# Performance work log

Measured on AMD Instinct MI355X. Metric: run time of the kernel, lower is better.

Reference implementation:

```python
import jax, jax.numpy as jnp
import numpy as np

B, S, D, H, DK, DFF, L = 4, 1024, 1024, 16, 64, 4096, 128

def setup_inputs() -> dict:
    key = jax.random.key(0)
    ks = jax.random.split(key, 20)
    stdv = 1.0 / np.sqrt(D)
    u = lambda k, shape, s=stdv: jax.random.uniform(k, shape, jnp.float32, -s, s)
    x = jax.random.normal(ks[0], (B, S, D), jnp.float32)
    causal = jnp.triu(jnp.ones((S, S), bool), 1)          # True = masked
    attn_mask = jnp.broadcast_to(causal, (B, S, S))
    return {
        "x": x,
        "attn_mask": attn_mask,
        "W_q": u(ks[1], (H * DK, D)), "b_q": jnp.zeros((H * DK,)),
        "W_k": u(ks[2], (H * DK, D)), "b_k": jnp.zeros((H * DK,)),
        "W_v": u(ks[3], (H * DK, D)), "b_v": jnp.zeros((H * DK,)),
        "W_o": u(ks[4], (D, H * DK)), "b_o": jnp.zeros((D,)),
        "W_rel": u(ks[5], (2 * L + 1, DK), 1.0 / np.sqrt(DK)),
        "ln1_alpha": jnp.ones((D,)), "ln1_bias": jnp.zeros((D,)),
        "ln2_alpha": jnp.ones((D,)), "ln2_bias": jnp.zeros((D,)),
        "W1": u(ks[6], (DFF, D)), "b1": jnp.zeros((DFF,)),
        "W2": u(ks[7], (D, DFF)), "b2": jnp.zeros((D,)),
    }

def _layer_norm(x, alpha, bias, eps=1e-5):
    # Faithful to source: (x - mean) / (std + eps), std is biased (unbiased=False)
    m = jnp.mean(x, axis=-1, keepdims=True)
    std = jnp.sqrt(jnp.mean((x - m) ** 2, axis=-1, keepdims=True))
    return alpha * (x - m) / (std + eps) + bias

def reference(x, attn_mask, W_q, b_q, W_k, b_k, W_v, b_v, W_o, b_o, W_rel,
              ln1_alpha, ln1_bias, ln2_alpha, ln2_bias, W1, b1, W2, b2):
    b, s, d = x.shape
    q = (x @ W_q.T + b_q).reshape(b, s, H, DK)
    k = (x @ W_k.T + b_k).reshape(b, s, H, DK)
    v = (x @ W_v.T + b_v).reshape(b, s, H, DK)
    # relative position bias table lookup -> [s, s, DK]
    idx = jnp.clip(jnp.arange(s)[:, None] - jnp.arange(s)[None, :], -L, L) + L
    pos = W_rel[idx]
    # NOTE: original uses rel_pos_k_emb for BOTH pos_key and pos_value (as in source).
    scores = jnp.einsum('bqnd,bknd->bnqk', q, k) + jnp.einsum('bqnd,qkd->bnqk', q, pos)
    scores = scores / np.sqrt(DK)
    scores = jnp.where(attn_mask[:, None, :, :], jnp.float32(-10000.0), scores)
    attn = jax.nn.softmax(scores, axis=-1)
    out = jnp.einsum('bnqk,bknd->bnqd', attn, v) + jnp.einsum('bnqk,qkd->bnqd', attn, pos)
    out = out.transpose(0, 2, 1, 3).reshape(b, s, H * DK)
    out = out @ W_o.T + b_o
    # post-LN transformer layer: LN(x + attn), then LN(h + FFN(h))
    h = _layer_norm(x + out, ln1_alpha, ln1_bias)
    f = jax.nn.relu(h @ W1.T + b1) @ W2.T + b2
    return _layer_norm(h + f, ln2_alpha, ln2_bias)
```

## Files before the change

kernel.cpp:

```cpp
#include <hip/hip_runtime.h>
#include <cmath>
#include <cstdint>

typedef __bf16 bf16;
typedef __bf16 bf16x8 __attribute__((ext_vector_type(8)));
typedef __bf16 bf16x4 __attribute__((ext_vector_type(4)));
typedef float f32x4 __attribute__((ext_vector_type(4)));

#define CEXP 0.1803368852f

__device__ __forceinline__ void async_ld16(const void* g, void* l) {
  __builtin_amdgcn_global_load_lds(
      (__attribute__((address_space(1))) void*)(uintptr_t)g,
      (__attribute__((address_space(3))) void*)l, 16, 0, 0);
}

__global__ __launch_bounds__(256) void cast_all(
    const float* __restrict__ x,  const float* __restrict__ wq, const float* __restrict__ wk,
    const float* __restrict__ wv, const float* __restrict__ wo, const float* __restrict__ w1,
    const float* __restrict__ w2,
    bf16* xb, bf16* wqb, bf16* wkb, bf16* wvb, bf16* wob, bf16* w1b, bf16* w2b)
{
  int i = blockIdx.x * 256 + threadIdx.x;
  const int M1 = 1 << 20, Q = 1 << 18;
  const float* src; bf16* dst; int off;
  if      (i < M1)            { src = x;  dst = xb;  off = i; }
  else if (i < M1 + Q)        { src = wq; dst = wqb; off = i - M1; }
  else if (i < M1 + 2 * Q)    { src = wk; dst = wkb; off = i - M1 - Q; }
  else if (i < M1 + 3 * Q)    { src = wv; dst = wvb; off = i - M1 - 2 * Q; }
  else if (i < M1 + 4 * Q)    { src = wo; dst = wob; off = i - M1 - 3 * Q; }
  else if (i < 3 * M1)        { src = w1; dst = w1b; off = i - M1 - 4 * Q; }
  else                        { src = w2; dst = w2b; off = i - 3 * M1; }
  float4 v = ((const float4*)src)[off];
  bf16x4 o; o[0]=(bf16)v.x; o[1]=(bf16)v.y; o[2]=(bf16)v.z; o[3]=(bf16)v.w;
  ((bf16x4*)dst)[off] = o;
}

template<int BM>
__device__ __forceinline__ void gemm_core(
    const bf16* __restrict__ A, const bf16* __restrict__ Bm, const float* __restrict__ bias,
    float* __restrict__ outF, bf16* __restrict__ outB,
    const float* __restrict__ residF, const bf16* __restrict__ residB,
    int N, int kld, int kbeg, int kend, int relu, bf16* As, bf16* Bs)
{
  constexpr int MI = BM / 32;
  const int tid  = threadIdx.x;
  const int wave = tid >> 6, lane = tid & 63;
  const int lr = lane & 15, lq = lane >> 4;
  const int bm = blockIdx.x * BM, bn = blockIdx.y * 128;
  const int wm = (wave >> 1) * (BM / 2), wn = (wave & 1) * 64;
  const int srow = lane >> 2, scol = (lane & 3) * 8;

  const f32x4 fz = {0.f, 0.f, 0.f, 0.f};
  f32x4 acc[MI][4];
#pragma unroll
  for (int i = 0; i < MI; i++)
#pragma unroll
    for (int j = 0; j < 4; j++) acc[i][j] = fz;

  auto issue = [&](int k0, int buf) {
    bf16* Ad = As + buf * (BM * 32);
    bf16* Bd = Bs + buf * (128 * 32);
    if (BM == 128) {
#pragma unroll
      for (int cc = 0; cc < 2; ++cc) {
        int c = wave * 2 + cc;
        async_ld16(A + (size_t)(bm + c * 16 + srow) * kld + k0 + scol, Ad + c * 512);
      }
    } else {
      async_ld16(A + (size_t)(bm + wave * 16 + srow) * kld + k0 + scol, Ad + wave * 512);
    }
#pragma unroll
    for (int cc = 0; cc < 2; ++cc) {
      int c = wave * 2 + cc;
      async_ld16(Bm + (size_t)(bn + c * 16 + srow) * kld + k0 + scol, Bd + c * 512);
    }
  };

  const int nit = (kend - kbeg) >> 5;
  issue(kbeg, 0);
  for (int i = 0; i < nit; i++) {
    __syncthreads();
    if (i + 1 < nit) issue(kbeg + (i + 1) * 32, (i + 1) & 1);
    const bf16* Ab = As + (i & 1) * (BM * 32);
    const bf16* Bb = Bs + (i & 1) * (128 * 32);
    bf16x8 af[MI], bfr[4];
#pragma unroll
    for (int mi = 0; mi < MI; mi++) af[mi]  = *(const bf16x8*)(Ab + (wm + mi*16 + lr)*32 + lq*8);
#pragma unroll
    for (int ni = 0; ni < 4; ni++) bfr[ni] = *(const bf16x8*)(Bb + (wn + ni*16 + lr)*32 + lq*8);
#pragma unroll
    for (int mi = 0; mi < MI; mi++)
#pragma unroll
      for (int ni = 0; ni < 4; ni++)
        acc[mi][ni] = __builtin_amdgcn_mfma_f32_16x16x32_bf16(af[mi], bfr[ni], acc[mi][ni], 0, 0, 0);
  }

#pragma unroll
  for (int ni = 0; ni < 4; ni++) {
    int n = bn + wn + ni*16 + lr;
    float bv = bias ? bias[n] : 0.0f;
#pragma unroll
    for (int mi = 0; mi < MI; mi++) {
#pragma unroll
      for (int r = 0; r < 4; r++) {
        int m = bm + wm + mi*16 + lq*4 + r;
        size_t idx = (size_t)m * N + n;
        float v = acc[mi][ni][r] + bv;
        if (relu) v = fmaxf(v, 0.0f);
        if (residF) v += residF[idx];
        if (residB) v += (float)residB[idx];
        if (outF) outF[idx] = v;
        else      outB[idx] = (bf16)v;
      }
    }
  }
}

__global__ __launch_bounds__(256) void gemm_qkv(
    const bf16* A, const bf16* Bq, const bf16* Bk, const bf16* Bv,
    const float* bq, const float* bk, const float* bv,
    bf16* Oq, bf16* Ok, bf16* Ov, int N, int K)
{
  __shared__ bf16 As[2 * 128 * 32];
  __shared__ bf16 Bs[2 * 128 * 32];
  const bf16* Bm  = blockIdx.z == 0 ? Bq : (blockIdx.z == 1 ? Bk : Bv);
  const float* bi = blockIdx.z == 0 ? bq : (blockIdx.z == 1 ? bk : bv);
  bf16* O         = blockIdx.z == 0 ? Oq : (blockIdx.z == 1 ? Ok : Ov);
  gemm_core<128>(A, Bm, bi, nullptr, O, nullptr, nullptr, N, K, 0, K, 0, As, Bs);
}

__device__ __forceinline__ void gemm256_core(
    const bf16* __restrict__ A, const bf16* __restrict__ Bm,
    const float* __restrict__ bias, bf16* __restrict__ outB, float* __restrict__ outF,
    int N, int kld, int kbeg, int kend, int relu, bf16* As, bf16* Bs)
{
  const int tid  = threadIdx.x;
  const int wave = tid >> 6, lane = tid & 63;
  const int lr = lane & 15, lq = lane >> 4;
  const int bm = blockIdx.x * 256, bn = blockIdx.y * 256;
  const int wm = (wave >> 2) * 128, wn = (wave & 3) * 64;

  const f32x4 fz = {0.f, 0.f, 0.f, 0.f};
  f32x4 acc[8][4];
#pragma unroll
  for (int i = 0; i < 8; ++i)
#pragma unroll
    for (int j = 0; j < 4; ++j) acc[i][j] = fz;

  int srow[4], scol[4];
#pragma unroll
  for (int L = 0; L < 4; ++L) {
    int cidx = L * 512 + wave * 64 + lane;
    srow[L] = cidx >> 3;
    scol[L] = ((cidx & 7) ^ (srow[L] & 7)) * 8;
  }

  auto issue = [&](int kt, int buf) {
    const int k0 = kbeg + kt * 64;
#pragma unroll
    for (int L = 0; L < 4; ++L)
      async_ld16(A + (size_t)(bm + srow[L]) * kld + k0 + scol[L],
                 As + buf * (256 * 64) + (L * 512 + wave * 64) * 8);
#pragma unroll
    for (int L = 0; L < 4; ++L)
      async_ld16(Bm + (size_t)(bn + srow[L]) * kld + k0 + scol[L],
                 Bs + buf * (256 * 64) + (L * 512 + wave * 64) * 8);
  };

  const int NT = (kend - kbeg) >> 6;
  issue(0, 0);
  issue(1, 1);
  asm volatile("s_waitcnt vmcnt(8)" ::: "memory");
  __builtin_amdgcn_sched_barrier(0);
  __builtin_amdgcn_s_barrier();

  for (int t = 0; t < NT; ++t) {
    const bf16* Ab = As + (t & 1) * (256 * 64);
    const bf16* Bb = Bs + (t & 1) * (256 * 64);
#pragma unroll
    for (int mh = 0; mh < 2; ++mh) {
      bf16x8 af[4][2];
#pragma unroll
      for (int mi = 0; mi < 4; ++mi) {
        int row = wm + mh * 64 + mi * 16 + lr;
#pragma unroll
        for (int ks = 0; ks < 2; ++ks)
          af[mi][ks] = *(const bf16x8*)(Ab + row * 64 + (((ks * 4 + lq) ^ (lr & 7)) * 8));
      }
#pragma unroll
      for (int nh = 0; nh < 2; ++nh) {
        bf16x8 bfr[2][2];
#pragma unroll
        for (int ni = 0; ni < 2; ++ni) {
          int row = wn + nh * 32 + ni * 16 + lr;
#pragma unroll
          for (int ks = 0; ks < 2; ++ks)
            bfr[ni][ks] = *(const bf16x8*)(Bb + row * 64 + (((ks * 4 + lq) ^ (lr & 7)) * 8));
        }
        __builtin_amdgcn_s_setprio(1);
#pragma unroll
        for (int mi = 0; mi < 4; ++mi)
#pragma unroll
          for (int ni = 0; ni < 2; ++ni)
#pragma unroll
            for (int ks = 0; ks < 2; ++ks)
              acc[mh * 4 + mi][nh * 2 + ni] = __builtin_amdgcn_mfma_f32_16x16x32_bf16(
                  af[mi][ks], bfr[ni][ks], acc[mh * 4 + mi][nh * 2 + ni], 0, 0, 0);
        __builtin_amdgcn_s_setprio(0);
      }
    }
    if (t + 1 == NT) break;
    asm volatile("s_waitcnt lgkmcnt(0)" ::: "memory");
    __builtin_amdgcn_sched_barrier(0);
    __builtin_amdgcn_s_barrier();
    if (t + 2 < NT) {
      issue(t + 2, t & 1);
      asm volatile("s_waitcnt vmcnt(8)" ::: "memory");
    } else {
      asm volatile("s_waitcnt vmcnt(0)" ::: "memory");
    }
    __builtin_amdgcn_sched_barrier(0);
    __builtin_amdgcn_s_barrier();
  }

#pragma unroll
  for (int mi8 = 0; mi8 < 8; ++mi8) {
#pragma unroll
    for (int ni4 = 0; ni4 < 4; ++ni4) {
      int n = bn + wn + ni4 * 16 + lr;
      float bv = bias ? bias[n] : 0.0f;
#pragma unroll
      for (int r = 0; r < 4; ++r) {
        int m = bm + wm + mi8 * 16 + lq * 4 + r;
        size_t idx = (size_t)m * N + n;
        float v = acc[mi8][ni4][r] + bv;
        if (relu) v = fmaxf(v, 0.0f);
        if (outF) outF[idx] = v;
        else      outB[idx] = (bf16)v;
      }
    }
  }
}

__global__ __launch_bounds__(512) void gemm256(
    const bf16* __restrict__ A, const bf16* __restrict__ Bm,
    const float* __restrict__ bias, bf16* __restrict__ outB,
    int N, int K, int relu)
{
  __shared__ __align__(16) bf16 As[2 * 256 * 64];
  __shared__ __align__(16) bf16 Bs[2 * 256 * 64];
  gemm256_core(A, Bm, bias, outB, nullptr, N, K, 0, K, relu, As, Bs);
}

__device__ __forceinline__ void gemm256x128_core(
    const bf16* __restrict__ A, const bf16* __restrict__ Bm, float* __restrict__ outF,
    int N, int kld, int kbeg, int kend, bf16* As, bf16* Bs)
{
  const int tid  = threadIdx.x;
  const int wave = tid >> 6, lane = tid & 63;
  const int lr = lane & 15, lq = lane >> 4;
  const int bm = blockIdx.x * 256, bn = blockIdx.y * 128;
  const int wm = (wave >> 1) * 64, wn = (wave & 1) * 64;

  const f32x4 fz = {0.f, 0.f, 0.f, 0.f};
  f32x4 acc[4][4];
#pragma unroll
  for (int i = 0; i < 4; ++i)
#pragma unroll
    for (int j = 0; j < 4; ++j) acc[i][j] = fz;

  int srowA[4], scolA[4], srowB[2], scolB[2];
#pragma unroll
  for (int L = 0; L < 4; ++L) {
    int cidx = L * 512 + wave * 64 + lane;
    srowA[L] = cidx >> 3;
    scolA[L] = ((cidx & 7) ^ (srowA[L] & 7)) * 8;
  }
#pragma unroll
  for (int L = 0; L < 2; ++L) {
    int cidx = L * 512 + wave * 64 + lane;
    srowB[L] = cidx >> 3;
    scolB[L] = ((cidx & 7) ^ (srowB[L] & 7)) * 8;
  }

  auto issue = [&](int kt, int buf) {
    const int k0 = kbeg + kt * 64;
#pragma unroll
    for (int L = 0; L < 4; ++L)
      async_ld16(A + (size_t)(bm + srowA[L]) * kld + k0 + scolA[L],
                 As + buf * (256 * 64) + (L * 512 + wave * 64) * 8);
#pragma unroll
    for (int L = 0; L < 2; ++L)
      async_ld16(Bm + (size_t)(bn + srowB[L]) * kld + k0 + scolB[L],
                 Bs + buf * (128 * 64) + (L * 512 + wave * 64) * 8);
  };

  const int NT = (kend - kbeg) >> 6;
  issue(0, 0);
  issue(1, 1);
  asm volatile("s_waitcnt vmcnt(6)" ::: "memory");
  __builtin_amdgcn_sched_barrier(0);
  __builtin_amdgcn_s_barrier();

  for (int t = 0; t < NT; ++t) {
    const bf16* Ab = As + (t & 1) * (256 * 64);
    const bf16* Bb = Bs + (t & 1) * (128 * 64);
    bf16x8 af[4][2], bfr[4][2];
#pragma unroll
    for (int mi = 0; mi < 4; ++mi) {
      int row = wm + mi * 16 + lr;
#pragma unroll
      for (int ks = 0; ks < 2; ++ks)
        af[mi][ks] = *(const bf16x8*)(Ab + row * 64 + (((ks * 4 + lq) ^ (lr & 7)) * 8));
    }
#pragma unroll
    for (int ni = 0; ni < 4; ++ni) {
      int row = wn + ni * 16 + lr;
#pragma unroll
      for (int ks = 0; ks < 2; ++ks)
        bfr[ni][ks] = *(const bf16x8*)(Bb + row * 64 + (((ks * 4 + lq) ^ (lr & 7)) * 8));
    }
    __builtin_amdgcn_s_setprio(1);
#pragma unroll
    for (int mi = 0; mi < 4; ++mi)
#pragma unroll
      for (int ni = 0; ni < 4; ++ni)
#pragma unroll
        for (int ks = 0; ks < 2; ++ks)
          acc[mi][ni] = __builtin_amdgcn_mfma_f32_16x16x32_bf16(
              af[mi][ks], bfr[ni][ks], acc[mi][ni], 0, 0, 0);
    __builtin_amdgcn_s_setprio(0);

    if (t + 1 == NT) break;
    asm volatile("s_waitcnt lgkmcnt(0)" ::: "memory");
    __builtin_amdgcn_sched_barrier(0);
    __builtin_amdgcn_s_barrier();
    if (t + 2 < NT) {
      issue(t + 2, t & 1);
      asm volatile("s_waitcnt vmcnt(6)" ::: "memory");
    } else {
      asm volatile("s_waitcnt vmcnt(0)" ::: "memory");
    }
    __builtin_amdgcn_sched_barrier(0);
    __builtin_amdgcn_s_barrier();
  }

#pragma unroll
  for (int mi = 0; mi < 4; ++mi) {
#pragma unroll
    for (int ni = 0; ni < 4; ++ni) {
      int n = bn + wn + ni * 16 + lr;
#pragma unroll
      for (int r = 0; r < 4; ++r) {
        int m = bm + wm + mi * 16 + lq * 4 + r;
        outF[(size_t)m * N + n] = acc[mi][ni][r];
      }
    }
  }
}

__global__ __launch_bounds__(512) void gemm256x128_splitk(
    const bf16* __restrict__ A, const bf16* __restrict__ Bm,
    float* p0, float* p1, int N, int kld, int kchunk)
{
  __shared__ __align__(16) bf16 As[2 * 256 * 64];
  __shared__ __align__(16) bf16 Bs[2 * 128 * 64];
  const int z = blockIdx.z;
  float* part = z == 0 ? p0 : p1;
  gemm256x128_core(A, Bm, part, N, kld, z * kchunk, (z + 1) * kchunk, As, Bs);
}

__global__ __launch_bounds__(256) void transpose_v(const bf16* __restrict__ V, bf16* __restrict__ Vt) {
  __shared__ bf16 t[64][72];
  const int tid = threadIdx.x;
  const int sblk = blockIdx.x;
  const int bh = blockIdx.y;
  const int b = bh >> 4, h = bh & 15;
  const int sr = tid >> 2, dc = (tid & 3) * 16;
  const bf16* src = V + ((size_t)(b * 1024 + sblk * 64 + sr)) * 1024 + h * 64 + dc;
  bf16x8 r0 = *(const bf16x8*)src;
  bf16x8 r1 = *(const bf16x8*)(src + 8);
  *(bf16x8*)(&t[sr][dc]) = r0;
  *(bf16x8*)(&t[sr][dc + 8]) = r1;
  __syncthreads();
  const int dr = tid >> 2, sc = (tid & 3) * 16;
  bf16 o[16];
#pragma unroll
  for (int j = 0; j < 16; j++) o[j] = t[sc + j][dr];
  bf16* dst = Vt + ((size_t)(bh * 64 + dr)) * 1024 + sblk * 64 + sc;
  *(bf16x8*)dst = *(bf16x8*)&o[0];
  *(bf16x8*)(dst + 8) = *(bf16x8*)&o[8];
}

#define S_LEN 1024
#define ROWSTR 1024

__global__ __launch_bounds__(256) void attn_kernel(
    const bf16* __restrict__ Qg, const bf16* __restrict__ Kg, const bf16* __restrict__ Vt,
    const float* __restrict__ Wrel, bf16* __restrict__ Og)
{
  __shared__ __align__(16) bf16 hist[64][136];
  __shared__ __align__(16) bf16 rel_s[64][132];
  __shared__ __align__(16) bf16 ovl[8704];
  bf16* V_T  = ovl;
  bf16* Pb   = ovl + 4096;
  bf16* Wst  = ovl;
  bf16* Wr_t = ovl;
  float* lbuf = (float*)rel_s;
  float* hbuf = lbuf + 256;

  const int tid = threadIdx.x;
  const int wave = tid >> 6, lane = tid & 63;
  const int lr = lane & 15, lq = lane >> 4;
  const int qblk = 15 - blockIdx.y;
  const int bh = blockIdx.x;
  const int b = bh >> 4, h = bh & 15;
  const int q0 = qblk * 64;
  const int T = qblk + 1;
  const int nearStart = (T > 3) ? T - 3 : 0;
  const size_t rowbase = (size_t)b * S_LEN * ROWSTR + h * 64;
  const size_t vtbase = (size_t)(bh * 64) * 1024;
  const f32x4 fz = {0.f, 0.f, 0.f, 0.f};

  for (int e = tid; e < 2048; e += 256) {
    float4 v = ((const float4*)(Wrel + 8192))[e];
    bf16x4 o; o[0]=(bf16)v.x; o[1]=(bf16)v.y; o[2]=(bf16)v.z; o[3]=(bf16)v.w;
    ((bf16x4*)Wst)[e] = o;
  }
  {
    uint4 z4 = {0u, 0u, 0u, 0u};
    for (int e = tid; e < 1088; e += 256) ((uint4*)hist)[e] = z4;
  }

  bf16x8 qf[4][2];
#pragma unroll
  for (int qt = 0; qt < 4; qt++)
#pragma unroll
    for (int c = 0; c < 2; c++)
      qf[qt][c] = *(const bf16x8*)(Qg + rowbase + (size_t)(q0 + qt*16 + lr) * ROWSTR + c*32 + lq*8);

  bf16x8 wb[2];
#pragma unroll
  for (int c = 0; c < 2; c++)
#pragma unroll
    for (int j = 0; j < 8; j++)
      wb[c][j] = (bf16)Wrel[(size_t)256 * 64 + c*32 + lq*8 + j];

  __syncthreads();

#pragma unroll
  for (int tt = 0; tt < 2; ++tt)
#pragma unroll
    for (int qt = 0; qt < 4; ++qt) {
      f32x4 a = fz;
#pragma unroll
      for (int c = 0; c < 2; c++) {
        bf16x8 wf = *(const bf16x8*)(Wst + (wave*32 + tt*16 + lr) * 64 + c*32 + lq*8);
        a = __builtin_amdgcn_mfma_f32_16x16x32_bf16(wf, qf[qt][c], a, 0, 0, 0);
      }
      bf16x4 pk; pk[0]=(bf16)(a[0]*CEXP); pk[1]=(bf16)(a[1]*CEXP);
                 pk[2]=(bf16)(a[2]*CEXP); pk[3]=(bf16)(a[3]*CEXP);
      *(bf16x4*)(&rel_s[qt*16 + lr][wave*32 + tt*16 + lq*4]) = pk;
    }
  {
    f32x4 a = fz;
#pragma unroll
    for (int c = 0; c < 2; c++)
      a = __builtin_amdgcn_mfma_f32_16x16x32_bf16(wb[c], qf[wave][c], a, 0, 0, 0);
    if (lq == 0) rel_s[wave*16 + lr][128] = (bf16)(a[0]*CEXP);
  }
  __syncthreads();

  float relc[4];
#pragma unroll
  for (int qt = 0; qt < 4; qt++) relc[qt] = (float)rel_s[qt*16 + lr][128];

  float l_p[4] = {0.f,0.f,0.f,0.f}, h_p[4] = {0.f,0.f,0.f,0.f};
  f32x4 acc_o[4];
#pragma unroll
  for (int dt = 0; dt < 4; dt++) acc_o[dt] = fz;

  const int vd1 = tid >> 3;
  const int vj  = (tid & 7) ^ (vd1 & 7);
  const int krow = 16 * wave + lr;

  uint4 va, vb, va2, vb2;
  bf16x8 kf0, kf1, kn0, kn1;
  {
    const bf16* vp = Vt + vtbase + (size_t)vd1 * 1024 + vj * 8;
    va = *(const uint4*)vp; vb = *(const uint4*)(vp + 32 * 1024);
    const bf16* kp = Kg + rowbase + (size_t)krow * ROWSTR + lq*8;
    kf0 = *(const bf16x8*)kp; kf1 = *(const bf16x8*)(kp + 32);
  }

  for (int kt = 0; kt < T; ++kt) {
    const int k0 = kt * 64;

    f32x4 sc[4];
#pragma unroll
    for (int qt = 0; qt < 4; qt++) {
      sc[qt] = __builtin_amdgcn_mfma_f32_16x16x32_bf16(kf0, qf[qt][0], fz, 0, 0, 0);
      sc[qt] = __builtin_amdgcn_mfma_f32_16x16x32_bf16(kf1, qf[qt][1], sc[qt], 0, 0, 0);
    }
    if (kt + 1 < T) {
      const bf16* vp = Vt + vtbase + (size_t)vd1 * 1024 + k0 + 64 + vj * 8;
      va2 = *(const uint4*)vp; vb2 = *(const uint4*)(vp + 32 * 1024);
      const bf16* kp = Kg + rowbase + (size_t)(k0 + 64 + krow) * ROWSTR + lq*8;
      kn0 = *(const bf16x8*)kp; kn1 = *(const bf16x8*)(kp + 32);
    }

    float pw[4][4];
    if (kt < nearStart) {
#pragma unroll
      for (int qt = 0; qt < 4; qt++) {
#pragma unroll
        for (int r = 0; r < 4; r++) pw[qt][r] = exp2f(fmaf(sc[qt][r], CEXP, relc[qt]));
        float s4 = pw[qt][0] + pw[qt][1] + pw[qt][2] + pw[qt][3];
        l_p[qt] += s4; h_p[qt] += s4;
      }
    } else {
#pragma unroll
      for (int qt = 0; qt < 4; qt++) {
        int qg = q0 + qt*16 + lr;
#pragma unroll
        for (int r = 0; r < 4; r++) {
          int kg = k0 + 16*wave + lq*4 + r;
          float p = 0.0f;
          if (kg <= qg) {
            int t = qg - kg; int tc = t > 128 ? 128 : t;
            p = exp2f(fmaf(sc[qt][r], CEXP, (float)rel_s[qt*16 + lr][tc]));
            l_p[qt] += p;
            if (t >= 128) h_p[qt] += p;
            else          hist[qt*16 + lr][t] = (bf16)p;
          }
          pw[qt][r] = p;
        }
      }
    }

    __syncthreads();
    *(uint4*)(V_T + tid * 8) = va;
    *(uint4*)(V_T + (tid + 256) * 8) = vb;
#pragma unroll
    for (int qt = 0; qt < 4; qt++) {
      bf16x4 pk; pk[0]=(bf16)pw[qt][0]; pk[1]=(bf16)pw[qt][1];
                 pk[2]=(bf16)pw[qt][2]; pk[3]=(bf16)pw[qt][3];
      *(bf16x4*)(Pb + (qt*16 + lr) * 72 + 16*wave + lq*4) = pk;
    }
    __syncthreads();

#pragma unroll
    for (int c = 0; c < 2; c++) {
      bf16x8 pf = *(const bf16x8*)(Pb + (16*wave + lr) * 72 + c*32 + lq*8);
#pragma unroll
      for (int dt = 0; dt < 4; dt++) {
        int vd = dt*16 + lr;
        int jx = (c*4 + lq) ^ (vd & 7);
        bf16x8 vf = *(const bf16x8*)(V_T + ((vd << 3) + jx) * 8);
        acc_o[dt] = __builtin_amdgcn_mfma_f32_16x16x32_bf16(pf, vf, acc_o[dt], 0, 0, 0);
      }
    }
    kf0 = kn0; kf1 = kn1; va = va2; vb = vb2;
  }

#pragma unroll
  for (int qt = 0; qt < 4; qt++) {
    l_p[qt] += __shfl_xor(l_p[qt], 16); l_p[qt] += __shfl_xor(l_p[qt], 32);
    h_p[qt] += __shfl_xor(h_p[qt], 16); h_p[qt] += __shfl_xor(h_p[qt], 32);
  }
  __syncthreads();
  if (lq == 0) {
#pragma unroll
    for (int qt = 0; qt < 4; qt++) {
      lbuf[wave*64 + qt*16 + lr] = l_p[qt];
      hbuf[wave*64 + qt*16 + lr] = h_p[qt];
    }
  }
  for (int e = tid; e < 64 * 128; e += 256) {
    int d = e >> 7, t = e & 127;
    Wr_t[d * 136 + t] = (bf16)Wrel[(size_t)(128 + t) * 64 + d];
  }
  __syncthreads();
#pragma unroll
  for (int c = 0; c < 4; c++) {
    bf16x8 hf = *(const bf16x8*)&hist[wave*16 + lr][c*32 + lq*8];
#pragma unroll
    for (int dt = 0; dt < 4; dt++) {
      bf16x8 wf = *(const bf16x8*)(Wr_t + (dt*16 + lr) * 136 + c*32 + lq*8);
      acc_o[dt] = __builtin_amdgcn_mfma_f32_16x16x32_bf16(hf, wf, acc_o[dt], 0, 0, 0);
    }
  }
  float l4[4], h4[4];
#pragma unroll
  for (int r = 0; r < 4; r++) {
    int q = wave*16 + lq*4 + r;
    l4[r] = lbuf[q] + lbuf[64+q] + lbuf[128+q] + lbuf[192+q];
    h4[r] = hbuf[q] + hbuf[64+q] + hbuf[128+q] + hbuf[192+q];
  }
#pragma unroll
  for (int dt = 0; dt < 4; dt++) {
    float wv = Wrel[(size_t)256 * 64 + dt*16 + lr];
#pragma unroll
    for (int r = 0; r < 4; r++) acc_o[dt][r] += h4[r] * wv;
  }
#pragma unroll
  for (int dt = 0; dt < 4; dt++)
#pragma unroll
    for (int r = 0; r < 4; r++) {
      int qg = q0 + wave*16 + lq*4 + r;
      Og[rowbase + (size_t)qg * ROWSTR + dt*16 + lr] = (bf16)(acc_o[dt][r] / l4[r]);
    }
}

__global__ __launch_bounds__(256) void ln_fuse(
    const float* __restrict__ pA, const float* __restrict__ pB,
    const float* __restrict__ pC, const float* __restrict__ pD,
    const float* __restrict__ bias,
    const float* __restrict__ residF, const bf16* __restrict__ residB,
    const float* __restrict__ alpha, const float* __restrict__ beta,
    float* __restrict__ outF, bf16* __restrict__ outB)
{
  const int row = blockIdx.x, tid = threadIdx.x;
  const int lane = tid & 63, wave = tid >> 6;
  const size_t base = (size_t)row * 1024;
  float4 v = ((const float4*)(pA + base))[tid];
  float4 v2 = ((const float4*)(pB + base))[tid];
  v.x += v2.x; v.y += v2.y; v.z += v2.z; v.w += v2.w;
  if (pC) {
    float4 v3 = ((const float4*)(pC + base))[tid];
    v.x += v3.x; v.y += v3.y; v.z += v3.z; v.w += v3.w;
  }
  if (pD) {
    float4 v4 = ((const float4*)(pD + base))[tid];
    v.x += v4.x; v.y += v4.y; v.z += v4.z; v.w += v4.w;
  }
  float4 bv = ((const float4*)bias)[tid];
  v.x += bv.x; v.y += bv.y; v.z += bv.z; v.w += bv.w;
  if (residF) {
    float4 rv = ((const float4*)(residF + base))[tid];
    v.x += rv.x; v.y += rv.y; v.z += rv.z; v.w += rv.w;
  }
  if (residB) {
    bf16x4 rv = ((const bf16x4*)(residB + base))[tid];
    v.x += (float)rv[0]; v.y += (float)rv[1]; v.z += (float)rv[2]; v.w += (float)rv[3];
  }
  float s  = v.x + v.y + v.z + v.w;
  float ss = v.x*v.x + v.y*v.y + v.z*v.z + v.w*v.w;
#pragma unroll
  for (int off = 32; off; off >>= 1) { s += __shfl_down(s, off); ss += __shfl_down(ss, off); }
  __shared__ float rs[4], rss[4];
  if (lane == 0) { rs[wave] = s; rss[wave] = ss; }
  __syncthreads();
  s  = rs[0] + rs[1] + rs[2] + rs[3];
  ss = rss[0] + rss[1] + rss[2] + rss[3];
  float mean = s * (1.0f / 1024.0f);
  float var  = ss * (1.0f / 1024.0f) - mean * mean;
  float inv  = 1.0f / (sqrtf(fmaxf(var, 0.0f)) + 1e-5f);
  float4 a = ((const float4*)alpha)[tid];
  float4 bb = ((const float4*)beta)[tid];
  float o0 = a.x * (v.x - mean) * inv + bb.x;
  float o1 = a.y * (v.y - mean) * inv + bb.y;
  float o2 = a.z * (v.z - mean) * inv + bb.z;
  float o3 = a.w * (v.w - mean) * inv + bb.w;
  if (outF) { float4 o = {o0, o1, o2, o3}; ((float4*)(outF + base))[tid] = o; }
  if (outB) { bf16x4 o; o[0]=(bf16)o0; o[1]=(bf16)o1; o[2]=(bf16)o2; o[3]=(bf16)o3;
              ((bf16x4*)(outB + base))[tid] = o; }
}

extern "C" void kernel_launch(void* const* d_in, const int* in_sizes, int n_in,
                              void* d_out, int out_size, void* d_ws, size_t ws_size,
                              hipStream_t stream) {
  (void)in_sizes; (void)n_in; (void)out_size; (void)ws_size;
  const int D = 1024, DFF = 4096;

  const float* x    = (const float*)d_in[0];
  const float* Wq   = (const float*)d_in[2];
  const float* bq   = (const float*)d_in[3];
  const float* Wk   = (const float*)d_in[4];
  const float* bk   = (const float*)d_in[5];
  const float* Wv   = (const float*)d_in[6];
  const float* bv   = (const float*)d_in[7];
  const float* Wo   = (const float*)d_in[8];
  const float* bo   = (const float*)d_in[9];
  const float* Wrel = (const float*)d_in[10];
  const float* g1   = (const float*)d_in[11];
  const float* be1  = (const float*)d_in[12];
  const float* g2   = (const float*)d_in[13];
  const float* be2  = (const float*)d_in[14];
  const float* W1   = (const float*)d_in[15];
  const float* b1   = (const float*)d_in[16];
  const float* W2   = (const float*)d_in[17];
  const float* b2   = (const float*)d_in[18];

  char* ws = (char*)d_ws;
  const size_t MB = 1024 * 1024;
  bf16*  xb   = (bf16*)(ws + 0);
  bf16*  Wqb  = (bf16*)(ws + 8  * MB);
  bf16*  Wkb  = (bf16*)(ws + 10 * MB);
  bf16*  Wvb  = (bf16*)(ws + 12 * MB);
  bf16*  Wob  = (bf16*)(ws + 14 * MB);
  bf16*  W1b  = (bf16*)(ws + 16 * MB);
  bf16*  W2b  = (bf16*)(ws + 24 * MB);
  bf16*  Qb   = (bf16*)(ws + 32 * MB);
  bf16*  Kb   = (bf16*)(ws + 40 * MB);
  bf16*  Vb   = (bf16*)(ws + 48 * MB);
  bf16*  Vt   = (bf16*)(ws + 56 * MB);
  bf16*  AOb  = (bf16*)(ws + 48 * MB);
  float* part = (float*)(ws + 64 * MB);
  bf16*  f1   = Qb;
  bf16*  hb   = xb;
  float* p0 = part;
  float* p1 = part + (size_t)4096 * 1024;

  cast_all<<<16384, 256, 0, stream>>>(x, Wq, Wk, Wv, Wo, W1, W2,
                                      xb, Wqb, Wkb, Wvb, Wob, W1b, W2b);

  gemm_qkv<<<dim3(32, 8, 3), 256, 0, stream>>>(xb, Wqb, Wkb, Wvb, bq, bk, bv, Qb, Kb, Vb, D, D);
  transpose_v<<<dim3(16, 64), 256, 0, stream>>>(Vb, Vt);
  attn_kernel<<<dim3(64, 16), 256, 0, stream>>>(Qb, Kb, Vt, Wrel, AOb);
  gemm256x128_splitk<<<dim3(16, 8, 2), 512, 0, stream>>>(AOb, Wob, p0, p1, D, D, 512);
  ln_fuse<<<4096, 256, 0, stream>>>(p0, p1, nullptr, nullptr,
                                    bo, x, nullptr, g1, be1, nullptr, hb);
  gemm256<<<dim3(16, 16), 512, 0, stream>>>(hb, W1b, b1, f1, DFF, D, 1);
  gemm256x128_splitk<<<dim3(16, 8, 2), 512, 0, stream>>>(f1, W2b, p0, p1, D, DFF, 2048);
  ln_fuse<<<4096, 256, 0, stream>>>(p0, p1, nullptr, nullptr,
                                    b2, nullptr, hb, g2, be2, (float*)d_out, nullptr);
}
```

Measured before the change: 373.8 us.

## Split long causal attention rows into separate far-key partial kernel

Adds an attn_far kernel that computes partial softmax numerators and row sums over the distant key blocks for query blocks 8-15, writing fp32 partial outputs and sums to workspace. The main attention kernel then starts from those partials and only iterates over the last 8 key blocks, which evens out per-block work across the causal triangle. The cost is an extra launch, fp32 partial writes and reads, and the two kernels running back to back instead of overlapping. It relies on the far region using no max subtraction, matching the existing unnormalized exp scheme.

```diff
diff --git a/kernel.cpp b/kernel.cpp
--- a/kernel.cpp
+++ b/kernel.cpp
@@ -396,9 +396,148 @@
 #define S_LEN 1024
 #define ROWSTR 1024
 
+__global__ __launch_bounds__(256) void attn_far(
+    const bf16* __restrict__ Qg, const bf16* __restrict__ Kg, const bf16* __restrict__ Vt,
+    const float* __restrict__ Wrel, float* __restrict__ Ofar, float* __restrict__ Lfar)
+{
+  __shared__ __align__(16) bf16 ovl[8704];
+  bf16* V_T = ovl;
+  bf16* Pb  = ovl + 4096;
+  __shared__ float relc_s[64];
+  __shared__ float lbuf[256];
+
+  const int tid = threadIdx.x;
+  const int wave = tid >> 6, lane = tid & 63;
+  const int lr = lane & 15, lq = lane >> 4;
+  const int qblk = 15 - blockIdx.y;
+  const int j = qblk - 8;
+  const int Tf = j + 1;
+  const int bh = blockIdx.x;
+  const int b = bh >> 4, h = bh & 15;
+  const int q0 = qblk * 64;
+  const size_t rowbase = (size_t)b * S_LEN * ROWSTR + h * 64;
+  const size_t vtbase = (size_t)(bh * 64) * 1024;
+  const f32x4 fz = {0.f, 0.f, 0.f, 0.f};
+
+  bf16x8 qf[4][2];
+#pragma unroll
+  for (int qt = 0; qt < 4; qt++)
+#pragma unroll
+    for (int c = 0; c < 2; c++)
+      qf[qt][c] = *(const bf16x8*)(Qg + rowbase + (size_t)(q0 + qt*16 + lr) * ROWSTR + c*32 + lq*8);
+
+  bf16x8 wb[2];
+#pragma unroll
+  for (int c = 0; c < 2; c++)
+#pragma unroll
+    for (int jj = 0; jj < 8; jj++)
+      wb[c][jj] = (bf16)Wrel[(size_t)256 * 64 + c*32 + lq*8 + jj];
+  {
+    f32x4 a = fz;
+#pragma unroll
+    for (int c = 0; c < 2; c++)
+      a = __builtin_amdgcn_mfma_f32_16x16x32_bf16(wb[c], qf[wave][c], a, 0, 0, 0);
+    if (lq == 0) relc_s[wave*16 + lr] = a[0] * CEXP;
+  }
+  __syncthreads();
+  float relc[4];
+#pragma unroll
+  for (int qt = 0; qt < 4; qt++) relc[qt] = relc_s[qt*16 + lr];
+
+  float l_p[4] = {0.f,0.f,0.f,0.f};
+  f32x4 acc_o[4];
+#pragma unroll
+  for (int dt = 0; dt < 4; dt++) acc_o[dt] = fz;
+
+  const int vd1 = tid >> 3;
+  const int vj  = (tid & 7) ^ (vd1 & 7);
+  const int krow = 16 * wave + lr;
+
+  uint4 va, vb, va2, vb2;
+  bf16x8 kf0, kf1, kn0, kn1;
+  {
+    const bf16* vp = Vt + vtbase + (size_t)vd1 * 1024 + vj * 8;
+    va = *(const uint4*)vp; vb = *(const uint4*)(vp + 32 * 1024);
+    const bf16* kp = Kg + rowbase + (size_t)krow * ROWSTR + lq*8;
+    kf0 = *(const bf16x8*)kp; kf1 = *(const bf16x8*)(kp + 32);
+  }
+
+  for (int kt = 0; kt < Tf; ++kt) {
+    const int k0 = kt * 64;
+    f32x4 sc[4];
+#pragma unroll
+    for (int qt = 0; qt < 4; qt++) {
+      sc[qt] = __builtin_amdgcn_mfma_f32_16x16x32_bf16(kf0, qf[qt][0], fz, 0, 0, 0);
+      sc[qt] = __builtin_amdgcn_mfma_f32_16x16x32_bf16(kf1, qf[qt][1], sc[qt], 0, 0, 0);
+    }
+    if (kt + 1 < Tf) {
+      const bf16* vp = Vt + vtbase + (size_t)vd1 * 1024 + k0 + 64 + vj * 8;
+      va2 = *(const uint4*)vp; vb2 = *(const uint4*)(vp + 32 * 1024);
+      const bf16* kp = Kg + rowbase + (size_t)(k0 + 64 + krow) * ROWSTR + lq*8;
+      kn0 = *(const bf16x8*)kp; kn1 = *(const bf16x8*)(kp + 32);
+    }
+
+    float pw[4][4];
+#pragma unroll
+    for (int qt = 0; qt < 4; qt++) {
+#pragma unroll
+      for (int r = 0; r < 4; r++) pw[qt][r] = exp2f(fmaf(sc[qt][r], CEXP, relc[qt]));
+      l_p[qt] += pw[qt][0] + pw[qt][1] + pw[qt][2] + pw[qt][3];
+    }
+
+    __syncthreads();
+    *(uint4*)(V_T + tid * 8) = va;
+    *(uint4*)(V_T + (tid + 256) * 8) = vb;
+#pragma unroll
+    for (int qt = 0; qt < 4; qt++) {
+      bf16x4 pk; pk[0]=(bf16)pw[qt][0]; pk[1]=(bf16)pw[qt][1];
+                 pk[2]=(bf16)pw[qt][2]; pk[3]=(bf16)pw[qt][3];
+      *(bf16x4*)(Pb + (qt*16 + lr) * 72 + 16*wave + lq*4) = pk;
+    }
+    __syncthreads();
+
+#pragma unroll
+    for (int c = 0; c < 2; c++) {
+      bf16x8 pf = *(const bf16x8*)(Pb + (16*wave + lr) * 72 + c*32 + lq*8);
+#pragma unroll
+      for (int dt = 0; dt < 4; dt++) {
+        int vd = dt*16 + lr;
+        int jx = (c*4 + lq) ^ (vd & 7);
+        bf16x8 vf = *(const bf16x8*)(V_T + ((vd << 3) + jx) * 8);
+        acc_o[dt] = __builtin_amdgcn_mfma_f32_16x16x32_bf16(pf, vf, acc_o[dt], 0, 0, 0);
+      }
+    }
+    kf0 = kn0; kf1 = kn1; va = va2; vb = vb2;
+  }
+
+#pragma unroll
+  for (int qt = 0; qt < 4; qt++) {
+    l_p[qt] += __shfl_xor(l_p[qt], 16); l_p[qt] += __shfl_xor(l_p[qt], 32);
+  }
+  if (lq == 0) {
+#pragma unroll
+    for (int qt = 0; qt < 4; qt++) lbuf[wave*64 + qt*16 + lr] = l_p[qt];
+  }
+  __syncthreads();
+  const size_t obase = ((size_t)(bh * 8 + j)) * 4096;
+#pragma unroll
+  for (int dt = 0; dt < 4; dt++)
+#pragma unroll
+    for (int r = 0; r < 4; r++)
+      Ofar[obase + (size_t)(wave*16 + lq*4 + r) * 64 + dt*16 + lr] = acc_o[dt][r];
+  if (lr == 0) {
+#pragma unroll
+    for (int r = 0; r < 4; r++) {
+      int q = wave*16 + lq*4 + r;
+      Lfar[(size_t)(bh * 8 + j) * 64 + q] = lbuf[q] + lbuf[64+q] + lbuf[128+q] + lbuf[192+q];
+    }
+  }
+}
+
 __global__ __launch_bounds__(256) void attn_kernel(
     const bf16* __restrict__ Qg, const bf16* __restrict__ Kg, const bf16* __restrict__ Vt,
-    const float* __restrict__ Wrel, bf16* __restrict__ Og)
+    const float* __restrict__ Wrel, bf16* __restrict__ Og,
+    const float* __restrict__ Ofar, const float* __restrict__ Lfar)
 {
   __shared__ __align__(16) bf16 hist[64][136];
   __shared__ __align__(16) bf16 rel_s[64][132];
@@ -418,6 +557,7 @@
   const int b = bh >> 4, h = bh & 15;
   const int q0 = qblk * 64;
   const int T = qblk + 1;
+  const int ktStart = (T > 8) ? T - 8 : 0;
   const int nearStart = (T > 3) ? T - 3 : 0;
   const size_t rowbase = (size_t)b * S_LEN * ROWSTR + h * 64;
   const size_t vtbase = (size_t)(bh * 64) * 1024;
@@ -444,8 +584,8 @@
 #pragma unroll
   for (int c = 0; c < 2; c++)
 #pragma unroll
-    for (int j = 0; j < 8; j++)
-      wb[c][j] = (bf16)Wrel[(size_t)256 * 64 + c*32 + lq*8 + j];
+    for (int jj = 0; jj < 8; jj++)
+      wb[c][jj] = (bf16)Wrel[(size_t)256 * 64 + c*32 + lq*8 + jj];
 
   __syncthreads();
 
@@ -480,23 +620,31 @@
   f32x4 acc_o[4];
 #pragma unroll
   for (int dt = 0; dt < 4; dt++) acc_o[dt] = fz;
+  if (ktStart > 0) {
+    const size_t obase = ((size_t)(bh * 8 + (qblk - 8))) * 4096;
+#pragma unroll
+    for (int dt = 0; dt < 4; dt++)
+#pragma unroll
+      for (int r = 0; r < 4; r++)
+        acc_o[dt][r] = Ofar[obase + (size_t)(wave*16 + lq*4 + r) * 64 + dt*16 + lr];
+  }
 
   const int vd1 = tid >> 3;
   const int vj  = (tid & 7) ^ (vd1 & 7);
   const int krow = 16 * wave + lr;
+  const int ks0 = ktStart * 64;
 
   uint4 va, vb, va2, vb2;
   bf16x8 kf0, kf1, kn0, kn1;
   {
-    const bf16* vp = Vt + vtbase + (size_t)vd1 * 1024 + vj * 8;
+    const bf16* vp = Vt + vtbase + (size_t)vd1 * 1024 + ks0 + vj * 8;
     va = *(const uint4*)vp; vb = *(const uint4*)(vp + 32 * 1024);
-    const bf16* kp = Kg + rowbase + (size_t)krow * ROWSTR + lq*8;
+    const bf16* kp = Kg + rowbase + (size_t)(ks0 + krow) * ROWSTR + lq*8;
     kf0 = *(const bf16x8*)kp; kf1 = *(const bf16x8*)(kp + 32);
   }
 
-  for (int kt = 0; kt < T; ++kt) {
+  for (int kt = ktStart; kt < T; ++kt) {
     const int k0 = kt * 64;
-
     f32x4 sc[4];
 #pragma unroll
     for (int qt = 0; qt < 4; qt++) {
@@ -597,6 +745,14 @@
     int q = wave*16 + lq*4 + r;
     l4[r] = lbuf[q] + lbuf[64+q] + lbuf[128+q] + lbuf[192+q];
     h4[r] = hbuf[q] + hbuf[64+q] + hbuf[128+q] + hbuf[192+q];
+  }
+  if (ktStart > 0) {
+#pragma unroll
+    for (int r = 0; r < 4; r++) {
+      int q = wave*16 + lq*4 + r;
+      float lf = Lfar[(size_t)(bh * 8 + (qblk - 8)) * 64 + q];
+      l4[r] += lf; h4[r] += lf;
+    }
   }
 #pragma unroll
   for (int dt = 0; dt < 4; dt++) {
@@ -712,13 +868,16 @@
   bf16*  hb   = xb;
   float* p0 = part;
   float* p1 = part + (size_t)4096 * 1024;
+  float* Ofar = (float*)(ws + 64 * MB);
+  float* Lfar = (float*)(ws + 72 * MB);
 
   cast_all<<<16384, 256, 0, stream>>>(x, Wq, Wk, Wv, Wo, W1, W2,
                                       xb, Wqb, Wkb, Wvb, Wob, W1b, W2b);
 
   gemm_qkv<<<dim3(32, 8, 3), 256, 0, stream>>>(xb, Wqb, Wkb, Wvb, bq, bk, bv, Qb, Kb, Vb, D, D);
   transpose_v<<<dim3(16, 64), 256, 0, stream>>>(Vb, Vt);
-  attn_kernel<<<dim3(64, 16), 256, 0, stream>>>(Qb, Kb, Vt, Wrel, AOb);
+  attn_far<<<dim3(64, 8), 256, 0, stream>>>(Qb, Kb, Vt, Wrel, Ofar, Lfar);
+  attn_kernel<<<dim3(64, 16), 256, 0, stream>>>(Qb, Kb, Vt, Wrel, AOb, Ofar, Lfar);
   gemm256x128_splitk<<<dim3(16, 8, 2), 512, 0, stream>>>(AOb, Wob, p0, p1, D, D, 512);
   ln_fuse<<<4096, 256, 0, stream>>>(p0, p1, nullptr, nullptr,
                                     bo, x, nullptr, g1, be1, nullptr, hb);
```

Measured after the change: 390.9 us. 1.05x slower.

## Rewrite QKV GEMM with BK=64, XOR-swizzled LDS, and deeper prefetch

Applied to the files above, without the earlier changes.

The QKV projection GEMM is now a dedicated kernel. It uses a 64-wide K tile, stores tiles in LDS with an XOR swizzle to avoid bank conflicts, and keeps two tiles in flight using explicit vmcnt waits and s_barrier. MFMA sections are wrapped in setprio. This should cut sync overhead per K step and improve overlap of global loads with compute, at the cost of doubling LDS use (64KB per block), which may lower occupancy.

```diff
diff --git a/kernel.cpp b/kernel.cpp
--- a/kernel.cpp
+++ b/kernel.cpp
@@ -36,98 +36,113 @@
   ((bf16x4*)dst)[off] = o;
 }
 
-template<int BM>
-__device__ __forceinline__ void gemm_core(
-    const bf16* __restrict__ A, const bf16* __restrict__ Bm, const float* __restrict__ bias,
-    float* __restrict__ outF, bf16* __restrict__ outB,
-    const float* __restrict__ residF, const bf16* __restrict__ residB,
-    int N, int kld, int kbeg, int kend, int relu, bf16* As, bf16* Bs)
+__global__ __launch_bounds__(256) void gemm128_qkv(
+    const bf16* __restrict__ A, const bf16* __restrict__ Bq, const bf16* __restrict__ Bk,
+    const bf16* __restrict__ Bv, const float* __restrict__ bq, const float* __restrict__ bk,
+    const float* __restrict__ bv, bf16* Oq, bf16* Ok, bf16* Ov, int N, int K)
 {
-  constexpr int MI = BM / 32;
+  __shared__ __align__(16) bf16 As[2 * 128 * 64];
+  __shared__ __align__(16) bf16 Bs[2 * 128 * 64];
+  const bf16* Bm  = blockIdx.z == 0 ? Bq : (blockIdx.z == 1 ? Bk : Bv);
+  const float* bi = blockIdx.z == 0 ? bq : (blockIdx.z == 1 ? bk : bv);
+  bf16* O         = blockIdx.z == 0 ? Oq : (blockIdx.z == 1 ? Ok : Ov);
+
   const int tid  = threadIdx.x;
   const int wave = tid >> 6, lane = tid & 63;
   const int lr = lane & 15, lq = lane >> 4;
-  const int bm = blockIdx.x * BM, bn = blockIdx.y * 128;
-  const int wm = (wave >> 1) * (BM / 2), wn = (wave & 1) * 64;
-  const int srow = lane >> 2, scol = (lane & 3) * 8;
+  const int bm = blockIdx.x * 128, bn = blockIdx.y * 128;
+  const int wm = (wave >> 1) * 64, wn = (wave & 1) * 64;
 
   const f32x4 fz = {0.f, 0.f, 0.f, 0.f};
-  f32x4 acc[MI][4];
-#pragma unroll
-  for (int i = 0; i < MI; i++)
-#pragma unroll
-    for (int j = 0; j < 4; j++) acc[i][j] = fz;
-
-  auto issue = [&](int k0, int buf) {
-    bf16* Ad = As + buf * (BM * 32);
-    bf16* Bd = Bs + buf * (128 * 32);
-    if (BM == 128) {
-#pragma unroll
-      for (int cc = 0; cc < 2; ++cc) {
-        int c = wave * 2 + cc;
-        async_ld16(A + (size_t)(bm + c * 16 + srow) * kld + k0 + scol, Ad + c * 512);
-      }
+  f32x4 acc[4][4];
+#pragma unroll
+  for (int i = 0; i < 4; ++i)
+#pragma unroll
+    for (int j = 0; j < 4; ++j) acc[i][j] = fz;
+
+  int srow[4], scol[4];
+#pragma unroll
+  for (int L = 0; L < 4; ++L) {
+    int cidx = L * 256 + wave * 64 + lane;
+    srow[L] = cidx >> 3;
+    scol[L] = ((cidx & 7) ^ (srow[L] & 7)) * 8;
+  }
+
+  auto issue = [&](int kt, int buf) {
+    const int k0 = kt * 64;
+#pragma unroll
+    for (int L = 0; L < 4; ++L)
+      async_ld16(A + (size_t)(bm + srow[L]) * K + k0 + scol[L],
+                 As + buf * (128 * 64) + (L * 256 + wave * 64) * 8);
+#pragma unroll
+    for (int L = 0; L < 4; ++L)
+      async_ld16(Bm + (size_t)(bn + srow[L]) * K + k0 + scol[L],
+                 Bs + buf * (128 * 64) + (L * 256 + wave * 64) * 8);
+  };
+
+  const int NT = K >> 6;
+  issue(0, 0);
+  issue(1, 1);
+  asm volatile("s_waitcnt vmcnt(8)" ::: "memory");
+  __builtin_amdgcn_sched_barrier(0);
+  __builtin_amdgcn_s_barrier();
+
+  for (int t = 0; t < NT; ++t) {
+    const bf16* Ab = As + (t & 1) * (128 * 64);
+    const bf16* Bb = Bs + (t & 1) * (128 * 64);
+    bf16x8 af[4][2], bfr[4][2];
+#pragma unroll
+    for (int mi = 0; mi < 4; ++mi) {
+      int row = wm + mi * 16 + lr;
+#pragma unroll
+      for (int ks = 0; ks < 2; ++ks)
+        af[mi][ks] = *(const bf16x8*)(Ab + row * 64 + (((ks * 4 + lq) ^ (lr & 7)) * 8));
+    }
+#pragma unroll
+    for (int ni = 0; ni < 4; ++ni) {
+      int row = wn + ni * 16 + lr;
+#pragma unroll
+      for (int ks = 0; ks < 2; ++ks)
+        bfr[ni][ks] = *(const bf16x8*)(Bb + row * 64 + (((ks * 4 + lq) ^ (lr & 7)) * 8));
+    }
+    __builtin_amdgcn_s_setprio(1);
+#pragma unroll
+    for (int mi = 0; mi < 4; ++mi)
+#pragma unroll
+      for (int ni = 0; ni < 4; ++ni)
+#pragma unroll
+        for (int ks = 0; ks < 2; ++ks)
+          acc[mi][ni] = __builtin_amdgcn_mfma_f32_16x16x32_bf16(
+              af[mi][ks], bfr[ni][ks], acc[mi][ni], 0, 0, 0);
+    __builtin_amdgcn_s_setprio(0);
+
+    if (t + 1 == NT) break;
+    asm volatile("s_waitcnt lgkmcnt(0)" ::: "memory");
+    __builtin_amdgcn_sched_barrier(0);
+    __builtin_amdgcn_s_barrier();
+    if (t + 2 < NT) {
+      issue(t + 2, t & 1);
+      asm volatile("s_waitcnt vmcnt(8)" ::: "memory");
     } else {
-      async_ld16(A + (size_t)(bm + wave * 16 + srow) * kld + k0 + scol, Ad + wave * 512);
-    }
-#pragma unroll
-    for (int cc = 0; cc < 2; ++cc) {
-      int c = wave * 2 + cc;
-      async_ld16(Bm + (size_t)(bn + c * 16 + srow) * kld + k0 + scol, Bd + c * 512);
-    }
-  };
-
-  const int nit = (kend - kbeg) >> 5;
-  issue(kbeg, 0);
-  for (int i = 0; i < nit; i++) {
-    __syncthreads();
-    if (i + 1 < nit) issue(kbeg + (i + 1) * 32, (i + 1) & 1);
-    const bf16* Ab = As + (i & 1) * (BM * 32);
-    const bf16* Bb = Bs + (i & 1) * (128 * 32);
-    bf16x8 af[MI], bfr[4];
-#pragma unroll
-    for (int mi = 0; mi < MI; mi++) af[mi]  = *(const bf16x8*)(Ab + (wm + mi*16 + lr)*32 + lq*8);
-#pragma unroll
-    for (int ni = 0; ni < 4; ni++) bfr[ni] = *(const bf16x8*)(Bb + (wn + ni*16 + lr)*32 + lq*8);
-#pragma unroll
-    for (int mi = 0; mi < MI; mi++)
-#pragma unroll
-      for (int ni = 0; ni < 4; ni++)
-        acc[mi][ni] = __builtin_amdgcn_mfma_f32_16x16x32_bf16(af[mi], bfr[ni], acc[mi][ni], 0, 0, 0);
-  }
-
-#pragma unroll
-  for (int ni = 0; ni < 4; ni++) {
-    int n = bn + wn + ni*16 + lr;
-    float bv = bias ? bias[n] : 0.0f;
-#pragma unroll
-    for (int mi = 0; mi < MI; mi++) {
-#pragma unroll
-      for (int r = 0; r < 4; r++) {
-        int m = bm + wm + mi*16 + lq*4 + r;
-        size_t idx = (size_t)m * N + n;
-        float v = acc[mi][ni][r] + bv;
-        if (relu) v = fmaxf(v, 0.0f);
-        if (residF) v += residF[idx];
-        if (residB) v += (float)residB[idx];
-        if (outF) outF[idx] = v;
-        else      outB[idx] = (bf16)v;
-      }
-    }
-  }
-}
-
-__global__ __launch_bounds__(256) void gemm_qkv(
-    const bf16* A, const bf16* Bq, const bf16* Bk, const bf16* Bv,
-    const float* bq, const float* bk, const float* bv,
-    bf16* Oq, bf16* Ok, bf16* Ov, int N, int K)
-{
-  __shared__ bf16 As[2 * 128 * 32];
-  __shared__ bf16 Bs[2 * 128 * 32];
-  const bf16* Bm  = blockIdx.z == 0 ? Bq : (blockIdx.z == 1 ? Bk : Bv);
-  const float* bi = blockIdx.z == 0 ? bq : (blockIdx.z == 1 ? bk : bv);
-  bf16* O         = blockIdx.z == 0 ? Oq : (blockIdx.z == 1 ? Ok : Ov);
-  gemm_core<128>(A, Bm, bi, nullptr, O, nullptr, nullptr, N, K, 0, K, 0, As, Bs);
+      asm volatile("s_waitcnt vmcnt(0)" ::: "memory");
+    }
+    __builtin_amdgcn_sched_barrier(0);
+    __builtin_amdgcn_s_barrier();
+  }
+
+#pragma unroll
+  for (int mi = 0; mi < 4; ++mi) {
+#pragma unroll
+    for (int ni = 0; ni < 4; ++ni) {
+      int n = bn + wn + ni * 16 + lr;
+      float bv2 = bi[n];
+#pragma unroll
+      for (int r = 0; r < 4; ++r) {
+        int m = bm + wm + mi * 16 + lq * 4 + r;
+        O[(size_t)m * N + n] = (bf16)(acc[mi][ni][r] + bv2);
+      }
+    }
+  }
 }
 
 __device__ __forceinline__ void gemm256_core(
@@ -716,7 +731,7 @@
   cast_all<<<16384, 256, 0, stream>>>(x, Wq, Wk, Wv, Wo, W1, W2,
                                       xb, Wqb, Wkb, Wvb, Wob, W1b, W2b);
 
-  gemm_qkv<<<dim3(32, 8, 3), 256, 0, stream>>>(xb, Wqb, Wkb, Wvb, bq, bk, bv, Qb, Kb, Vb, D, D);
+  gemm128_qkv<<<dim3(32, 8, 3), 256, 0, stream>>>(xb, Wqb, Wkb, Wvb, bq, bk, bv, Qb, Kb, Vb, D, D);
   transpose_v<<<dim3(16, 64), 256, 0, stream>>>(Vb, Vt);
   attn_kernel<<<dim3(64, 16), 256, 0, stream>>>(Qb, Kb, Vt, Wrel, AOb);
   gemm256x128_splitk<<<dim3(16, 8, 2), 512, 0, stream>>>(AOb, Wob, p0, p1, D, D, 512);
```

After: 377.8 us. No clear change (+1.1%).
